# Optimization experiments

Measured on AMD Instinct MI355X. Metric: run time of the kernel, lower is better.

The kernel has to match this reference:

```python
import jax, jax.numpy as jnp
import numpy as np

NUM_HEADS = 16
ROPE_BASE = 10000.0

def rotate_half(x):
    h = x.shape[-1] // 2
    return jnp.concatenate([-x[..., h:], x[..., :h]], axis=-1)

def setup_inputs() -> dict:
    key = jax.random.key(0)
    k1, k2, k3, k4 = jax.random.split(key, 4)
    B, T, H = 2, 2048, 1024
    hidden_state = jax.random.normal(k1, (B, T, H), dtype=jnp.float32)
    # right-padding mask: per-batch valid lengths
    lengths = jnp.array([2048, 1536], dtype=jnp.int32)
    attention_mask = (jnp.arange(T, dtype=jnp.int32)[None, :] < lengths[:, None]).astype(jnp.int32)
    s = 1.0 / np.sqrt(H)
    w_qkv = jax.random.normal(k2, (H, 3 * H), dtype=jnp.float32) * s
    b_qkv = jax.random.normal(k3, (3 * H,), dtype=jnp.float32) * 0.01
    w_out = jax.random.normal(k4, (H, H), dtype=jnp.float32) * s
    return {"hidden_state": hidden_state, "attention_mask": attention_mask,
            "w_qkv": w_qkv, "b_qkv": b_qkv, "w_out": w_out}

def reference(hidden_state, attention_mask, w_qkv, b_qkv, w_out):
    B, T, H = hidden_state.shape
    hd = H // NUM_HEADS
    qkv = hidden_state @ w_qkv + b_qkv                      # [B,T,3H]
    qkv = qkv.reshape(B, T, NUM_HEADS, 3 * hd).swapaxes(1, 2)  # [B,h,T,3d]
    q, k, v = qkv[..., :hd], qkv[..., hd:2 * hd], qkv[..., 2 * hd:]
    # rotary embedding (cache computed in fp32, as in torch module)
    inv_freq = 1.0 / (ROPE_BASE ** (jnp.arange(0, hd, 2, dtype=jnp.float32) / hd))
    t = jnp.arange(T, dtype=jnp.float32)
    freqs = jnp.outer(t, inv_freq)                          # [T, hd/2]
    emb = jnp.concatenate([freqs, freqs], axis=-1)          # [T, hd]
    cos = jnp.cos(emb)[None, None]                          # [1,1,T,hd]
    sin = jnp.sin(emb)[None, None]
    q = q * cos + rotate_half(q) * sin
    k = k * cos + rotate_half(k) * sin
    scale = 1.0 / jnp.sqrt(jnp.asarray(hd, dtype=q.dtype))
    scores = jnp.einsum('bhqd,bhkd->bhqk', q, k) * scale    # [B,h,T,T]
    causal = jnp.triu(jnp.ones((T, T), dtype=bool), k=1)    # True = masked (future)
    pad = (attention_mask == 0)[:, None, None, :]           # True = masked (padded key)
    mask = causal[None, None] | pad
    scores = jnp.where(mask, jnp.finfo(scores.dtype).min, scores)
    attn = jax.nn.softmax(scores, axis=-1)
    out = jnp.einsum('bhqk,bhkd->bhqd', attn, v)            # [B,h,T,d]
    out = out.swapaxes(1, 2).reshape(B, T, H)
    return out @ w_out
```

## Files before the change

kernel.cpp:

```cpp
#include <hip/hip_runtime.h>
#include <math.h>

typedef __attribute__((ext_vector_type(8))) short short8;
typedef __attribute__((ext_vector_type(4))) short short4v;
typedef __attribute__((ext_vector_type(4))) float floatx4;

#define T_SEQ 2048
#define NHEADS 16
#define HID 1024

#if __has_builtin(__builtin_amdgcn_mfma_f32_16x16x16bf16_1k)
#define MFMA16(a,b,c) __builtin_amdgcn_mfma_f32_16x16x16bf16_1k(a,b,c,0,0,0)
#elif __has_builtin(__builtin_amdgcn_mfma_f32_16x16x16_bf16)
#define MFMA16(a,b,c) __builtin_amdgcn_mfma_f32_16x16x16_bf16(a,b,c,0,0,0)
#else
#define MFMA16(a,b,c) (c)
#endif

#if __has_builtin(__builtin_amdgcn_exp2f)
#define EXP2F(x) __builtin_amdgcn_exp2f(x)
#else
#define EXP2F(x) exp2f(x)
#endif

__device__ __forceinline__ ushort f2b(float x){
  union { float f; unsigned u; } c; c.f = x;
  unsigned r = c.u + 0x7fffu + ((c.u >> 16) & 1u);
  return (ushort)(r >> 16);
}

__device__ __forceinline__ floatx4 fzero4(){
  floatx4 v; v[0]=0.f; v[1]=0.f; v[2]=0.f; v[3]=0.f; return v;
}

__device__ __forceinline__ void gl_lds16(const ushort* g, ushort* l){
  __builtin_amdgcn_global_load_lds(
      (const __attribute__((address_space(1))) void*)g,
      (__attribute__((address_space(3))) void*)l, 16, 0, 0);
}


__global__ __launch_bounds__(256) void prep(
    const float* __restrict__ hidden, const float* __restrict__ w_qkv,
    const float* __restrict__ w_out, const int* __restrict__ amask,
    ushort* __restrict__ hO, ushort* __restrict__ wqkvT, ushort* __restrict__ woutT,
    float2* __restrict__ cs, int* __restrict__ Lb)
{
  __shared__ __align__(16) char smem[32 * 33 * 4];
  int blk = blockIdx.x;
  int tid = threadIdx.x;

  if (blk < 4096){
    int i = blk * 256 + tid;
    float4 v = ((const float4*)hidden)[i];
    ushort4 o;
    o.x = f2b(v.x); o.y = f2b(v.y); o.z = f2b(v.z); o.w = f2b(v.w);
    ((ushort4*)hO)[i] = o;
  } else if (blk < 8192){
    const float* in; ushort* out; int R, C, bx, by;
    if (blk < 7168){
      int t = blk - 4096; bx = t % 96; by = t / 96;
      in = w_qkv; out = wqkvT; R = 1024; C = 3072;
    } else {
      int t = blk - 7168; bx = t & 31; by = t >> 5;
      in = w_out; out = woutT; R = 1024; C = 1024;
    }
    float (*tile)[33] = (float(*)[33])smem;
    int c0 = bx * 32, r0 = by * 32;
    int tx = tid & 31, ty = tid >> 5;
    #pragma unroll
    for (int i = 0; i < 4; i++){
      int r = ty + i * 8;
      tile[r][tx] = in[(size_t)(r0 + r) * C + c0 + tx];
    }
    __syncthreads();
    #pragma unroll
    for (int i = 0; i < 4; i++){
      int r = ty + i * 8;
      out[(size_t)(c0 + r) * R + r0 + tx] = f2b(tile[tx][r]);
    }
  } else if (blk < 8448){
    int idx = (blk - 8192) * 256 + tid;
    int t = idx >> 5, i = idx & 31;
    float invf = powf(10000.0f, -(float)i / 32.0f);
    float a = (float)t * invf;
    cs[idx] = make_float2(cosf(a), sinf(a));
  } else {
    int b = blk - 8448;
    int* red = (int*)smem;
    int s = 0;
    for (int i = tid; i < T_SEQ; i += 256) s += amask[b * T_SEQ + i];
    red[tid] = s; __syncthreads();
    for (int o = 128; o > 0; o >>= 1){
      if (tid < o) red[tid] += red[tid + o];
      __syncthreads();
    }
    if (tid == 0) Lb[b] = red[0];
  }
}


__global__ __launch_bounds__(768, 3) void gemm_qkv(
    const ushort* __restrict__ A, const ushort* __restrict__ Bt,
    const float* __restrict__ bias,
    ushort* __restrict__ qO, ushort* __restrict__ kO, ushort* __restrict__ vT,
    const float2* __restrict__ cs)
{
  __shared__ __align__(16) ushort As[3 * 16384];
  __shared__ __align__(16) ushort Bs[2 * 12288];
  int tid = threadIdx.x;
  int bid = blockIdx.x;
  int swz = (bid & 7) * 32 + (bid >> 3);
  int bm = swz >> 4, bn = swz & 15;
  int wave = tid >> 6, lane = tid & 63;
  int wm = wave & 3, wn = wave >> 2;
  int quad = lane >> 4, l15 = lane & 15, l7 = lane & 7;

  int lr3 = lane >> 3, sl = lane & 7;
  int gsl = sl ^ lr3;
  const ushort* gA = A  + (size_t)(bm * 256 + wave * 8 + lr3) * 1024 + (gsl << 3);
  const ushort* gB = Bt + (size_t)(bn * 192 + (wave - 8) * 8 + lr3) * 1024 + (gsl << 3);

  auto stageA = [&](int slot, int kt2){
    #pragma unroll
    for (int i = 0; i < 4; i++)
      gl_lds16(gA + (size_t)(i * 64) * 1024 + kt2 * 64,
               &As[slot * 16384 + i * 4096 + wave * 512]);
  };
  auto stageB = [&](int slot, int kt2){
    #pragma unroll
    for (int i = 0; i < 6; i++)
      gl_lds16(gB + (size_t)(i * 32) * 1024 + kt2 * 64,
               &Bs[slot * 12288 + i * 2048 + (wave - 8) * 512]);
  };

  int s0 = (quad ^ l7) << 3;
  int s1 = ((quad + 4) ^ l7) << 3;

  floatx4 acc[4][4];
  #pragma unroll
  for (int i = 0; i < 4; i++)
    #pragma unroll
    for (int j = 0; j < 4; j++) acc[i][j] = fzero4();

  if (tid < 512){ stageA(0, 0); stageA(1, 1); }
  else          { stageB(0, 0); }

  int aCur = 0, aStage = 2, bCur = 0;

  for (int kt = 0; kt < 16; ++kt){
    if (tid < 512){
      if (kt < 15) asm volatile("s_waitcnt vmcnt(4)" ::: "memory");
      else         asm volatile("s_waitcnt vmcnt(0)" ::: "memory");
    } else {
      asm volatile("s_waitcnt vmcnt(0)" ::: "memory");
    }
    __builtin_amdgcn_s_barrier();

    const ushort* Ac = &As[aCur * 16384];
    const ushort* Bc = &Bs[bCur * 12288];

    short8 af[4][2], bfr[2][2];
    #pragma unroll
    for (int mt = 0; mt < 4; mt++){
      int ro = (wm * 64 + mt * 16 + l15) * 64;
      af[mt][0] = *(const short8*)&Ac[ro + s0];
      af[mt][1] = *(const short8*)&Ac[ro + s1];
    }
    #pragma unroll
    for (int nt = 0; nt < 2; nt++){
      int ro = (wn * 64 + nt * 16 + l15) * 64;
      bfr[nt][0] = *(const short8*)&Bc[ro + s0];
      bfr[nt][1] = *(const short8*)&Bc[ro + s1];
    }
    if (tid < 512){ if (kt <= 13) stageA(aStage, kt + 2); }
    else          { if (kt <= 14) stageB(bCur ^ 1, kt + 1); }

    __builtin_amdgcn_s_setprio(1);
    #pragma unroll
    for (int mt = 0; mt < 4; mt++)
      #pragma unroll
      for (int nt = 0; nt < 2; nt++){
        acc[mt][nt] = __builtin_amdgcn_mfma_f32_16x16x32_bf16(af[mt][0], bfr[nt][0], acc[mt][nt], 0, 0, 0);
        acc[mt][nt] = __builtin_amdgcn_mfma_f32_16x16x32_bf16(af[mt][1], bfr[nt][1], acc[mt][nt], 0, 0, 0);
      }
    __builtin_amdgcn_s_setprio(0);

    short8 bfr2[2][2];
    #pragma unroll
    for (int nt = 0; nt < 2; nt++){
      int ro = (wn * 64 + (nt + 2) * 16 + l15) * 64;
      bfr2[nt][0] = *(const short8*)&Bc[ro + s0];
      bfr2[nt][1] = *(const short8*)&Bc[ro + s1];
    }
    __builtin_amdgcn_s_setprio(1);
    #pragma unroll
    for (int mt = 0; mt < 4; mt++)
      #pragma unroll
      for (int nt = 0; nt < 2; nt++){
        acc[mt][nt + 2] = __builtin_amdgcn_mfma_f32_16x16x32_bf16(af[mt][0], bfr2[nt][0], acc[mt][nt + 2], 0, 0, 0);
        acc[mt][nt + 2] = __builtin_amdgcn_mfma_f32_16x16x32_bf16(af[mt][1], bfr2[nt][1], acc[mt][nt + 2], 0, 0, 0);
      }
    __builtin_amdgcn_s_setprio(0);

    aCur   = (aCur   == 2) ? 0 : aCur + 1;
    aStage = (aStage == 2) ? 0 : aStage + 1;
    bCur ^= 1;
  }

  int g = bn * 3 + wn;
  int h = g / 3, comp = g - h * 3;

  if (comp == 2){
    #pragma unroll
    for (int nt = 0; nt < 4; nt++){
      int d = nt * 16 + l15;
      float bv = bias[g * 64 + d];
      #pragma unroll
      for (int mt = 0; mt < 4; mt++){
        int row = bm * 256 + wm * 64 + mt * 16 + quad * 4;
        int t = row & (T_SEQ - 1), b_ = row >> 11;
        int u = ((t >> 2) & 3) * 2 + ((t >> 5) & 1);
        int off = (t & ~63) + u * 8 + ((t >> 4) & 1) * 4;
        ushort4 o;
        o.x = f2b(acc[mt][nt][0] + bv);
        o.y = f2b(acc[mt][nt][1] + bv);
        o.z = f2b(acc[mt][nt][2] + bv);
        o.w = f2b(acc[mt][nt][3] + bv);
        *(ushort4*)&vT[(size_t)((b_ * NHEADS + h) * 64 + d) * T_SEQ + off] = o;
      }
    }
  } else {
    ushort* outP = (comp == 0) ? qO : kO;
    float qs = (comp == 0) ? 0.125f * 1.44269504089f : 1.0f;
    float bv[4], bp[4];
    #pragma unroll
    for (int nt = 0; nt < 4; nt++){
      bv[nt] = bias[g * 64 + nt * 16 + l15];
      bp[nt] = bias[g * 64 + ((nt * 16 + l15) ^ 32)];
    }
    #pragma unroll
    for (int mt = 0; mt < 4; mt++)
      #pragma unroll
      for (int r = 0; r < 4; r++){
        int row = bm * 256 + wm * 64 + mt * 16 + quad * 4 + r;
        int t = row & (T_SEQ - 1), b_ = row >> 11;
        float2 c0 = cs[t * 32 + l15];
        float2 c1 = cs[t * 32 + 16 + l15];
        size_t base = (size_t)((b_ * NHEADS + h) * T_SEQ + t) * 64 + l15;
        #pragma unroll
        for (int nt = 0; nt < 4; nt++){
          float cvv = (nt & 1) ? c1.x : c0.x;
          float svv = (nt & 1) ? c1.y : c0.y;
          float sgn = (nt < 2) ? -1.0f : 1.0f;
          float val = acc[mt][nt][r] + bv[nt];
          float pv  = acc[mt][nt ^ 2][r] + bp[nt];
          outP[base + nt * 16] = f2b((val * cvv + sgn * pv * svv) * qs);
        }
      }
  }
}


__global__ __launch_bounds__(256) void attn(
    const ushort* __restrict__ qB, const ushort* __restrict__ kB,
    const ushort* __restrict__ vTB, const int* __restrict__ Lb,
    ushort* __restrict__ oB)
{
  __shared__ __align__(16) ushort SH[2][8192];
  int tid = threadIdx.x;
  int bh = blockIdx.x;
  int qt = 31 - blockIdx.y;
  int b = bh >> 4, h = bh & 15;
  int wave = tid >> 6, lane = tid & 63;
  int quad = lane >> 4, l15 = lane & 15;
  int q0 = qt * 64;
  int L = Lb[b];

  const ushort* Qb  = qB + (size_t)bh * T_SEQ * 64;
  const ushort* Kb  = kB + (size_t)bh * T_SEQ * 64;
  const ushort* VtB = vTB + (size_t)bh * 64 * T_SEQ;

  int qrow = q0 + wave * 16 + l15;
  short8 qf0 = *(const short8*)&Qb[(size_t)qrow * 64 + quad * 8];
  short8 qf1 = *(const short8*)&Qb[(size_t)qrow * 64 + 32 + quad * 8];

  int lr = lane >> 3, ch = lane & 7;
  int sw = (ch ^ lr) * 8;
  int l7 = l15 & 7;

  float l_i = 0.f;
  floatx4 oacc[4];
  #pragma unroll
  for (int nt = 0; nt < 4; nt++) oacc[nt] = fzero4();

  int lastkb = qt;
  int lkb2 = (L - 1) >> 6;
  if (lkb2 < lastkb) lastkb = lkb2;

  auto stageKV = [&](int kb, int buf){
    int k0 = kb * 64;
    const ushort* gK = &Kb[(size_t)(k0 + wave * 16 + lr) * 64 + sw];
    gl_lds16(gK,          &SH[buf][(wave * 16) * 64]);
    gl_lds16(gK + 8 * 64, &SH[buf][(wave * 16 + 8) * 64]);
    const ushort* gV = &VtB[(size_t)(wave * 16 + lr) * T_SEQ + k0 + sw];
    gl_lds16(gV,             &SH[buf][4096 + (wave * 16) * 64]);
    gl_lds16(gV + 8 * T_SEQ, &SH[buf][4096 + (wave * 16 + 8) * 64]);
  };

  stageKV(0, 0);
  __syncthreads();

  for (int kb = 0; kb <= lastkb; ++kb){
    int cur = kb & 1;
    if (kb < lastkb) stageKV(kb + 1, cur ^ 1);
    const ushort* Ks = &SH[cur][0];
    const ushort* Vt = &SH[cur][4096];
    int k0 = kb * 64;

    floatx4 sacc[4];
    #pragma unroll
    for (int e = 0; e < 4; e++){
      short8 kf0 = *(const short8*)&Ks[(e * 16 + l15) * 64 + ((quad ^ l7) * 8)];
      short8 kf1 = *(const short8*)&Ks[(e * 16 + l15) * 64 + (((quad | 4) ^ l7) * 8)];
      floatx4 z = fzero4();
      z = __builtin_amdgcn_mfma_f32_16x16x32_bf16(kf0, qf0, z, 0, 0, 0);
      z = __builtin_amdgcn_mfma_f32_16x16x32_bf16(kf1, qf1, z, 0, 0, 0);
      sacc[e] = z;
    }

    float p[4][4];
    bool needm = (kb == qt) || (k0 + 64 > L);
    if (needm){
      #pragma unroll
      for (int e = 0; e < 4; e++)
        #pragma unroll
        for (int r = 0; r < 4; r++){
          int key = k0 + e * 16 + quad * 4 + r;
          float ev = EXP2F(sacc[e][r]);
          p[e][r] = (key <= qrow && key < L) ? ev : 0.f;
        }
    } else {
      #pragma unroll
      for (int e = 0; e < 4; e++)
        #pragma unroll
        for (int r = 0; r < 4; r++) p[e][r] = EXP2F(sacc[e][r]);
    }
    float s0 = 0.f, s1 = 0.f, s2 = 0.f, s3 = 0.f;
    #pragma unroll
    for (int e = 0; e < 4; e++){
      s0 += p[e][0]; s1 += p[e][1]; s2 += p[e][2]; s3 += p[e][3];
    }
    l_i += (s0 + s1) + (s2 + s3);

    short4v pf[4];
    #pragma unroll
    for (int e = 0; e < 4; e++){
      union { unsigned u[2]; short4v v; } pk;
      pk.u[0] = (__float_as_uint(p[e][1]) & 0xffff0000u) | (__float_as_uint(p[e][0]) >> 16);
      pk.u[1] = (__float_as_uint(p[e][3]) & 0xffff0000u) | (__float_as_uint(p[e][2]) >> 16);
      pf[e] = pk.v;
    }

    #pragma unroll
    for (int nt = 0; nt < 4; nt++){
      #pragma unroll
      for (int ep = 0; ep < 2; ep++){
        short8 v2 = *(const short8*)&Vt[(nt * 16 + l15) * 64 + (((quad * 2 + ep) ^ l7) * 8)];
        short4v vf0, vf1;
        vf0[0] = v2[0]; vf0[1] = v2[1]; vf0[2] = v2[2]; vf0[3] = v2[3];
        vf1[0] = v2[4]; vf1[1] = v2[5]; vf1[2] = v2[6]; vf1[3] = v2[7];
        oacc[nt] = MFMA16(vf0, pf[ep * 2],     oacc[nt]);
        oacc[nt] = MFMA16(vf1, pf[ep * 2 + 1], oacc[nt]);
      }
    }
    __syncthreads();
  }

  l_i += __shfl_xor(l_i, 16);
  l_i += __shfl_xor(l_i, 32);
  float inv = 1.f / l_i;

  ushort (*Ot)[80] = (ushort(*)[80])&SH[0][0];
  #pragma unroll
  for (int nt = 0; nt < 4; nt++){
    ushort4 o;
    o.x = f2b(oacc[nt][0] * inv);
    o.y = f2b(oacc[nt][1] * inv);
    o.z = f2b(oacc[nt][2] * inv);
    o.w = f2b(oacc[nt][3] * inv);
    *(ushort4*)&Ot[wave * 16 + l15][nt * 16 + quad * 4] = o;
  }
  __syncthreads();
  int r = tid >> 2, c = (tid & 3) * 16;
  short8 o0 = *(const short8*)&Ot[r][c];
  short8 o1 = *(const short8*)&Ot[r][c + 8];
  ushort* dst = &oB[(size_t)((b * T_SEQ + q0 + r) * NHEADS + h) * 64 + c];
  *(short8*)dst = o0;
  *(short8*)(dst + 8) = o1;
}


__global__ __launch_bounds__(512, 2) void gemm_out_k(
    const ushort* __restrict__ A, const ushort* __restrict__ Bt,
    float* __restrict__ out)
{
  __shared__ __align__(16) ushort As[3 * 16384];
  __shared__ __align__(16) ushort Bs[2 * 4096];
  int tid = threadIdx.x;
  int bid = blockIdx.x;
  int swz = (bid & 7) * 32 + (bid >> 3);
  int bm = swz >> 4, bn = swz & 15;
  int wave = tid >> 6, lane = tid & 63;
  int wm = wave >> 1, wn = wave & 1;
  int quad = lane >> 4, l15 = lane & 15, l7 = lane & 7;

  int lr3 = lane >> 3, sl = lane & 7;
  int gsl = sl ^ lr3;
  const ushort* gA = A + (size_t)(bm * 256 + wave * 8 + lr3) * 1024 + (gsl << 3);
  int rB = tid >> 3;
  int gslB = (tid & 7) ^ (rB & 7);
  const ushort* gB = Bt + (size_t)(bn * 64 + rB) * 1024 + (gslB << 3);

  auto stageA = [&](int slot, int kt2){
    #pragma unroll
    for (int i = 0; i < 4; i++)
      gl_lds16(gA + (size_t)(i * 64) * 1024 + kt2 * 64,
               &As[slot * 16384 + i * 4096 + wave * 512]);
  };
  auto stageB = [&](int slot, int kt2){
    gl_lds16(gB + kt2 * 64, &Bs[slot * 4096 + wave * 512]);
  };

  int s0 = (quad ^ l7) << 3;
  int s1 = ((quad + 4) ^ l7) << 3;

  floatx4 acc[4][2];
  #pragma unroll
  for (int i = 0; i < 4; i++){ acc[i][0] = fzero4(); acc[i][1] = fzero4(); }

  stageB(0, 0);
  stageA(0, 0);
  stageA(1, 1);
  int aCur = 0, aStage = 2, bCur = 0;

  for (int kt = 0; kt < 16; ++kt){
    if (kt < 15) asm volatile("s_waitcnt vmcnt(4)" ::: "memory");
    else         asm volatile("s_waitcnt vmcnt(0)" ::: "memory");
    __builtin_amdgcn_s_barrier();

    const ushort* Ac = &As[aCur * 16384];
    const ushort* Bc = &Bs[bCur * 4096];

    short8 af[4][2], bf0[2], bf1[2];
    #pragma unroll
    for (int mt = 0; mt < 4; mt++){
      int ro = (wm * 64 + mt * 16 + l15) * 64;
      af[mt][0] = *(const short8*)&Ac[ro + s0];
      af[mt][1] = *(const short8*)&Ac[ro + s1];
    }
    {
      int ro = (wn * 32 + l15) * 64;
      bf0[0] = *(const short8*)&Bc[ro + s0];
      bf0[1] = *(const short8*)&Bc[ro + s1];
    }
    if (kt <= 14) stageB(bCur ^ 1, kt + 1);

    __builtin_amdgcn_s_setprio(1);
    #pragma unroll
    for (int mt = 0; mt < 4; mt++){
      acc[mt][0] = __builtin_amdgcn_mfma_f32_16x16x32_bf16(af[mt][0], bf0[0], acc[mt][0], 0, 0, 0);
      acc[mt][0] = __builtin_amdgcn_mfma_f32_16x16x32_bf16(af[mt][1], bf0[1], acc[mt][0], 0, 0, 0);
    }
    __builtin_amdgcn_s_setprio(0);

    {
      int ro = (wn * 32 + 16 + l15) * 64;
      bf1[0] = *(const short8*)&Bc[ro + s0];
      bf1[1] = *(const short8*)&Bc[ro + s1];
    }
    if (kt <= 13) stageA(aStage, kt + 2);

    __builtin_amdgcn_s_setprio(1);
    #pragma unroll
    for (int mt = 0; mt < 4; mt++){
      acc[mt][1] = __builtin_amdgcn_mfma_f32_16x16x32_bf16(af[mt][0], bf1[0], acc[mt][1], 0, 0, 0);
      acc[mt][1] = __builtin_amdgcn_mfma_f32_16x16x32_bf16(af[mt][1], bf1[1], acc[mt][1], 0, 0, 0);
    }
    __builtin_amdgcn_s_setprio(0);

    aCur   = (aCur   == 2) ? 0 : aCur + 1;
    aStage = (aStage == 2) ? 0 : aStage + 1;
    bCur ^= 1;
  }

  #pragma unroll
  for (int nt = 0; nt < 2; nt++){
    int n = bn * 64 + wn * 32 + nt * 16 + l15;
    #pragma unroll
    for (int mt = 0; mt < 4; mt++)
      #pragma unroll
      for (int r = 0; r < 4; r++){
        int row = bm * 256 + wm * 64 + mt * 16 + quad * 4 + r;
        out[(size_t)row * 1024 + n] = acc[mt][nt][r];
      }
  }
}


extern "C" void kernel_launch(void* const* d_in, const int* in_sizes, int n_in,
                              void* d_out, int out_size, void* d_ws, size_t ws_size,
                              hipStream_t stream)
{
  const float* hidden = (const float*)d_in[0];
  const int*   amask  = (const int*)d_in[1];
  const float* w_qkv  = (const float*)d_in[2];
  const float* b_qkv  = (const float*)d_in[3];
  const float* w_out  = (const float*)d_in[4];
  float* out = (float*)d_out;

  char* ws = (char*)d_ws;
  ushort* hO    = (ushort*)(ws);
  ushort* wqkvT = (ushort*)(ws + 8388608);
  ushort* woutT = (ushort*)(ws + 14680064);
  ushort* qB    = (ushort*)(ws + 16777216);
  ushort* kB    = (ushort*)(ws + 25165824);
  ushort* vT    = (ushort*)(ws + 33554432);
  float2* cs    = (float2*)(ws + 41943040);
  int*    Lb    = (int*)(ws + 42467328);

  prep<<<8450, 256, 0, stream>>>(hidden, w_qkv, w_out, amask, hO, wqkvT, woutT, cs, Lb);
  gemm_qkv<<<dim3(256), 768, 0, stream>>>(hO, wqkvT, b_qkv, qB, kB, vT, cs);
  attn<<<dim3(32, 32), 256, 0, stream>>>(qB, kB, vT, Lb, hO );
  gemm_out_k<<<dim3(256), 512, 0, stream>>>(hO, woutT, out);
}
```

Measured before the change: 163.8 us.

## Split GEMM K-step into two halves with extra barriers around MFMA clusters

Reorganizes the QKV projection GEMM inner loop so that each K tile is processed in two halves (s0 then s1) across all four N subtiles, instead of splitting by N subtiles. The A and B global-to-LDS staging are moved to different halves, and extra workgroup barriers are added around each MFMA cluster to keep waves in lockstep, ping-pong style. The aim is to spread the global loads out, overlap them with MFMA work, and reduce register pressure from fragments. The extra barriers add synchronization cost per iteration.

```diff
diff --git a/kernel.cpp b/kernel.cpp
--- a/kernel.cpp
+++ b/kernel.cpp
@@ -160,47 +160,39 @@
     const ushort* Ac = &As[aCur * 16384];
     const ushort* Bc = &Bs[bCur * 12288];
 
-    short8 af[4][2], bfr[2][2];
-    #pragma unroll
-    for (int mt = 0; mt < 4; mt++){
-      int ro = (wm * 64 + mt * 16 + l15) * 64;
-      af[mt][0] = *(const short8*)&Ac[ro + s0];
-      af[mt][1] = *(const short8*)&Ac[ro + s1];
-    }
-    #pragma unroll
-    for (int nt = 0; nt < 2; nt++){
-      int ro = (wn * 64 + nt * 16 + l15) * 64;
-      bfr[nt][0] = *(const short8*)&Bc[ro + s0];
-      bfr[nt][1] = *(const short8*)&Bc[ro + s1];
-    }
-    if (tid < 512){ if (kt <= 13) stageA(aStage, kt + 2); }
-    else          { if (kt <= 14) stageB(bCur ^ 1, kt + 1); }
-
+    short8 af[4], bf[4];
+
+    #pragma unroll
+    for (int mt = 0; mt < 4; mt++)
+      af[mt] = *(const short8*)&Ac[(wm * 64 + mt * 16 + l15) * 64 + s0];
+    #pragma unroll
+    for (int nt = 0; nt < 4; nt++)
+      bf[nt] = *(const short8*)&Bc[(wn * 64 + nt * 16 + l15) * 64 + s0];
+    if (tid < 512 && kt <= 13) stageA(aStage, kt + 2);
+    __builtin_amdgcn_s_barrier();
     __builtin_amdgcn_s_setprio(1);
     #pragma unroll
     for (int mt = 0; mt < 4; mt++)
       #pragma unroll
-      for (int nt = 0; nt < 2; nt++){
-        acc[mt][nt] = __builtin_amdgcn_mfma_f32_16x16x32_bf16(af[mt][0], bfr[nt][0], acc[mt][nt], 0, 0, 0);
-        acc[mt][nt] = __builtin_amdgcn_mfma_f32_16x16x32_bf16(af[mt][1], bfr[nt][1], acc[mt][nt], 0, 0, 0);
-      }
+      for (int nt = 0; nt < 4; nt++)
+        acc[mt][nt] = __builtin_amdgcn_mfma_f32_16x16x32_bf16(af[mt], bf[nt], acc[mt][nt], 0, 0, 0);
     __builtin_amdgcn_s_setprio(0);
-
-    short8 bfr2[2][2];
-    #pragma unroll
-    for (int nt = 0; nt < 2; nt++){
-      int ro = (wn * 64 + (nt + 2) * 16 + l15) * 64;
-      bfr2[nt][0] = *(const short8*)&Bc[ro + s0];
-      bfr2[nt][1] = *(const short8*)&Bc[ro + s1];
-    }
+    __builtin_amdgcn_s_barrier();
+
+    #pragma unroll
+    for (int mt = 0; mt < 4; mt++)
+      af[mt] = *(const short8*)&Ac[(wm * 64 + mt * 16 + l15) * 64 + s1];
+    #pragma unroll
+    for (int nt = 0; nt < 4; nt++)
+      bf[nt] = *(const short8*)&Bc[(wn * 64 + nt * 16 + l15) * 64 + s1];
+    if (tid >= 512 && kt <= 14) stageB(bCur ^ 1, kt + 1);
+    __builtin_amdgcn_s_barrier();
     __builtin_amdgcn_s_setprio(1);
     #pragma unroll
     for (int mt = 0; mt < 4; mt++)
       #pragma unroll
-      for (int nt = 0; nt < 2; nt++){
-        acc[mt][nt + 2] = __builtin_amdgcn_mfma_f32_16x16x32_bf16(af[mt][0], bfr2[nt][0], acc[mt][nt + 2], 0, 0, 0);
-        acc[mt][nt + 2] = __builtin_amdgcn_mfma_f32_16x16x32_bf16(af[mt][1], bfr2[nt][1], acc[mt][nt + 2], 0, 0, 0);
-      }
+      for (int nt = 0; nt < 4; nt++)
+        acc[mt][nt] = __builtin_amdgcn_mfma_f32_16x16x32_bf16(af[mt], bf[nt], acc[mt][nt], 0, 0, 0);
     __builtin_amdgcn_s_setprio(0);
 
     aCur   = (aCur   == 2) ? 0 : aCur + 1;
```

Result: no change. 167.0 us (+2.0%).

## Process two query row groups per wave in attention, halving block size

Applied to the files above, without the earlier changes.

The attention kernel now uses 2 waves of 128 threads instead of 4, and each wave handles 32 query rows (two 16-row groups) rather than 16. Each K and V fragment read from LDS is reused across both groups, which halves LDS read traffic per MFMA. The causal-mask check is now made per 16-row group. In exchange, each thread holds more accumulator registers and each block has fewer waves for hiding latency, which may lower occupancy.

```diff
diff --git a/kernel.cpp b/kernel.cpp
--- a/kernel.cpp
+++ b/kernel.cpp
@@ -262,7 +262,7 @@
 }
 
 
-__global__ __launch_bounds__(256) void attn(
+__global__ __launch_bounds__(128) void attn(
     const ushort* __restrict__ qB, const ushort* __restrict__ kB,
     const ushort* __restrict__ vTB, const int* __restrict__ Lb,
     ushort* __restrict__ oB)
@@ -281,18 +281,24 @@
   const ushort* Kb  = kB + (size_t)bh * T_SEQ * 64;
   const ushort* VtB = vTB + (size_t)bh * 64 * T_SEQ;
 
-  int qrow = q0 + wave * 16 + l15;
-  short8 qf0 = *(const short8*)&Qb[(size_t)qrow * 64 + quad * 8];
-  short8 qf1 = *(const short8*)&Qb[(size_t)qrow * 64 + 32 + quad * 8];
+  int qbase = q0 + wave * 32;
+  short8 qf[2][2];
+  #pragma unroll
+  for (int g = 0; g < 2; g++){
+    qf[g][0] = *(const short8*)&Qb[(size_t)(qbase + g * 16 + l15) * 64 + quad * 8];
+    qf[g][1] = *(const short8*)&Qb[(size_t)(qbase + g * 16 + l15) * 64 + 32 + quad * 8];
+  }
 
   int lr = lane >> 3, ch = lane & 7;
   int sw = (ch ^ lr) * 8;
   int l7 = l15 & 7;
 
-  float l_i = 0.f;
-  floatx4 oacc[4];
-  #pragma unroll
-  for (int nt = 0; nt < 4; nt++) oacc[nt] = fzero4();
+  float l_i[2] = {0.f, 0.f};
+  floatx4 oacc[2][4];
+  #pragma unroll
+  for (int g = 0; g < 2; g++)
+    #pragma unroll
+    for (int nt = 0; nt < 4; nt++) oacc[g][nt] = fzero4();
 
   int lastkb = qt;
   int lkb2 = (L - 1) >> 6;
@@ -300,12 +306,14 @@
 
   auto stageKV = [&](int kb, int buf){
     int k0 = kb * 64;
-    const ushort* gK = &Kb[(size_t)(k0 + wave * 16 + lr) * 64 + sw];
-    gl_lds16(gK,          &SH[buf][(wave * 16) * 64]);
-    gl_lds16(gK + 8 * 64, &SH[buf][(wave * 16 + 8) * 64]);
-    const ushort* gV = &VtB[(size_t)(wave * 16 + lr) * T_SEQ + k0 + sw];
-    gl_lds16(gV,             &SH[buf][4096 + (wave * 16) * 64]);
-    gl_lds16(gV + 8 * T_SEQ, &SH[buf][4096 + (wave * 16 + 8) * 64]);
+    const ushort* gK = &Kb[(size_t)(k0 + wave * 32 + lr) * 64 + sw];
+    #pragma unroll
+    for (int i = 0; i < 4; i++)
+      gl_lds16(gK + i * 8 * 64, &SH[buf][(wave * 32 + i * 8) * 64]);
+    const ushort* gV = &VtB[(size_t)(wave * 32 + lr) * T_SEQ + k0 + sw];
+    #pragma unroll
+    for (int i = 0; i < 4; i++)
+      gl_lds16(gV + (size_t)(i * 8) * T_SEQ, &SH[buf][4096 + (wave * 32 + i * 8) * 64]);
   };
 
   stageKV(0, 0);
@@ -318,48 +326,54 @@
     const ushort* Vt = &SH[cur][4096];
     int k0 = kb * 64;
 
-    floatx4 sacc[4];
+    floatx4 sacc[2][4];
     #pragma unroll
     for (int e = 0; e < 4; e++){
       short8 kf0 = *(const short8*)&Ks[(e * 16 + l15) * 64 + ((quad ^ l7) * 8)];
       short8 kf1 = *(const short8*)&Ks[(e * 16 + l15) * 64 + (((quad | 4) ^ l7) * 8)];
-      floatx4 z = fzero4();
-      z = __builtin_amdgcn_mfma_f32_16x16x32_bf16(kf0, qf0, z, 0, 0, 0);
-      z = __builtin_amdgcn_mfma_f32_16x16x32_bf16(kf1, qf1, z, 0, 0, 0);
-      sacc[e] = z;
-    }
-
-    float p[4][4];
-    bool needm = (kb == qt) || (k0 + 64 > L);
-    if (needm){
-      #pragma unroll
-      for (int e = 0; e < 4; e++)
+      #pragma unroll
+      for (int g = 0; g < 2; g++){
+        floatx4 z = fzero4();
+        z = __builtin_amdgcn_mfma_f32_16x16x32_bf16(kf0, qf[g][0], z, 0, 0, 0);
+        z = __builtin_amdgcn_mfma_f32_16x16x32_bf16(kf1, qf[g][1], z, 0, 0, 0);
+        sacc[g][e] = z;
+      }
+    }
+
+    short4v pf[2][4];
+    #pragma unroll
+    for (int g = 0; g < 2; g++){
+      int qrow = qbase + g * 16 + l15;
+      float p[4][4];
+      bool needm = (k0 + 63 > qbase + g * 16) || (k0 + 64 > L);
+      if (needm){
         #pragma unroll
-        for (int r = 0; r < 4; r++){
-          int key = k0 + e * 16 + quad * 4 + r;
-          float ev = EXP2F(sacc[e][r]);
-          p[e][r] = (key <= qrow && key < L) ? ev : 0.f;
-        }
-    } else {
-      #pragma unroll
-      for (int e = 0; e < 4; e++)
+        for (int e = 0; e < 4; e++)
+          #pragma unroll
+          for (int r = 0; r < 4; r++){
+            int key = k0 + e * 16 + quad * 4 + r;
+            float ev = EXP2F(sacc[g][e][r]);
+            p[e][r] = (key <= qrow && key < L) ? ev : 0.f;
+          }
+      } else {
         #pragma unroll
-        for (int r = 0; r < 4; r++) p[e][r] = EXP2F(sacc[e][r]);
-    }
-    float s0 = 0.f, s1 = 0.f, s2 = 0.f, s3 = 0.f;
-    #pragma unroll
-    for (int e = 0; e < 4; e++){
-      s0 += p[e][0]; s1 += p[e][1]; s2 += p[e][2]; s3 += p[e][3];
-    }
-    l_i += (s0 + s1) + (s2 + s3);
-
-    short4v pf[4];
-    #pragma unroll
-    for (int e = 0; e < 4; e++){
-      union { unsigned u[2]; short4v v; } pk;
-      pk.u[0] = (__float_as_uint(p[e][1]) & 0xffff0000u) | (__float_as_uint(p[e][0]) >> 16);
-      pk.u[1] = (__float_as_uint(p[e][3]) & 0xffff0000u) | (__float_as_uint(p[e][2]) >> 16);
-      pf[e] = pk.v;
+        for (int e = 0; e < 4; e++)
+          #pragma unroll
+          for (int r = 0; r < 4; r++) p[e][r] = EXP2F(sacc[g][e][r]);
+      }
+      float s0 = 0.f, s1 = 0.f, s2 = 0.f, s3 = 0.f;
+      #pragma unroll
+      for (int e = 0; e < 4; e++){
+        s0 += p[e][0]; s1 += p[e][1]; s2 += p[e][2]; s3 += p[e][3];
+      }
+      l_i[g] += (s0 + s1) + (s2 + s3);
+      #pragma unroll
+      for (int e = 0; e < 4; e++){
+        union { unsigned u[2]; short4v v; } pk;
+        pk.u[0] = (__float_as_uint(p[e][1]) & 0xffff0000u) | (__float_as_uint(p[e][0]) >> 16);
+        pk.u[1] = (__float_as_uint(p[e][3]) & 0xffff0000u) | (__float_as_uint(p[e][2]) >> 16);
+        pf[g][e] = pk.v;
+      }
     }
 
     #pragma unroll
@@ -370,34 +384,48 @@
         short4v vf0, vf1;
         vf0[0] = v2[0]; vf0[1] = v2[1]; vf0[2] = v2[2]; vf0[3] = v2[3];
         vf1[0] = v2[4]; vf1[1] = v2[5]; vf1[2] = v2[6]; vf1[3] = v2[7];
-        oacc[nt] = MFMA16(vf0, pf[ep * 2],     oacc[nt]);
-        oacc[nt] = MFMA16(vf1, pf[ep * 2 + 1], oacc[nt]);
+        #pragma unroll
+        for (int g = 0; g < 2; g++){
+          oacc[g][nt] = MFMA16(vf0, pf[g][ep * 2],     oacc[g][nt]);
+          oacc[g][nt] = MFMA16(vf1, pf[g][ep * 2 + 1], oacc[g][nt]);
+        }
       }
     }
     __syncthreads();
   }
 
-  l_i += __shfl_xor(l_i, 16);
-  l_i += __shfl_xor(l_i, 32);
-  float inv = 1.f / l_i;
+  #pragma unroll
+  for (int g = 0; g < 2; g++){
+    l_i[g] += __shfl_xor(l_i[g], 16);
+    l_i[g] += __shfl_xor(l_i[g], 32);
+  }
+  float inv0 = 1.f / l_i[0], inv1 = 1.f / l_i[1];
 
   ushort (*Ot)[80] = (ushort(*)[80])&SH[0][0];
   #pragma unroll
-  for (int nt = 0; nt < 4; nt++){
-    ushort4 o;
-    o.x = f2b(oacc[nt][0] * inv);
-    o.y = f2b(oacc[nt][1] * inv);
-    o.z = f2b(oacc[nt][2] * inv);
-    o.w = f2b(oacc[nt][3] * inv);
-    *(ushort4*)&Ot[wave * 16 + l15][nt * 16 + quad * 4] = o;
+  for (int g = 0; g < 2; g++){
+    float inv = g ? inv1 : inv0;
+    #pragma unroll
+    for (int nt = 0; nt < 4; nt++){
+      ushort4 o;
+      o.x = f2b(oacc[g][nt][0] * inv);
+      o.y = f2b(oacc[g][nt][1] * inv);
+      o.z = f2b(oacc[g][nt][2] * inv);
+      o.w = f2b(oacc[g][nt][3] * inv);
+      *(ushort4*)&Ot[wave * 32 + g * 16 + l15][nt * 16 + quad * 4] = o;
+    }
   }
   __syncthreads();
-  int r = tid >> 2, c = (tid & 3) * 16;
+  int r = tid >> 1, c = (tid & 1) * 32;
   short8 o0 = *(const short8*)&Ot[r][c];
   short8 o1 = *(const short8*)&Ot[r][c + 8];
+  short8 o2 = *(const short8*)&Ot[r][c + 16];
+  short8 o3 = *(const short8*)&Ot[r][c + 24];
   ushort* dst = &oB[(size_t)((b * T_SEQ + q0 + r) * NHEADS + h) * 64 + c];
   *(short8*)dst = o0;
   *(short8*)(dst + 8) = o1;
+  *(short8*)(dst + 16) = o2;
+  *(short8*)(dst + 24) = o3;
 }
 
 
@@ -531,6 +559,6 @@
 
   prep<<<8450, 256, 0, stream>>>(hidden, w_qkv, w_out, amask, hO, wqkvT, woutT, cs, Lb);
   gemm_qkv<<<dim3(256), 768, 0, stream>>>(hO, wqkvT, b_qkv, qB, kB, vT, cs);
-  attn<<<dim3(32, 32), 256, 0, stream>>>(qB, kB, vT, Lb, hO );
+  attn<<<dim3(32, 32), 128, 0, stream>>>(qB, kB, vT, Lb, hO );
   gemm_out_k<<<dim3(256), 512, 0, stream>>>(hO, woutT, out);
 }
```

New measurement: 178.8 us. 1.09x slower.
